# Performance work log

Hardware: AMD Instinct MI355X
Metric: run time of the kernel (lower is better)

The kernel has to match this reference:

```python
import jax, jax.numpy as jnp
import numpy as np

B, V, H, W, C = 2, 4, 120, 160, 96
N_VOX = 200000
GRID = 128
VOXEL_SIZE = 0.05
DEPTH_MIN = 0.1 / VOXEL_SIZE   # 2.0 (voxel units)
DEPTH_MAX = 4.0 / VOXEL_SIZE   # 80.0 (voxel units)
STEP = 0.5                     # ray increment = voxel_size/2, in voxel units
N_STEPS = int((DEPTH_MAX - DEPTH_MIN) / STEP)  # 156


def setup_inputs() -> dict:
    key = jax.random.key(0)
    kf, kc = jax.random.split(key)
    feats = jax.random.normal(kf, (B, V, H, W, C), dtype=jnp.float32)
    # batch-sorted sparse voxel coords [N,4] = (b, x, y, z)
    xyz = jax.random.randint(kc, (N_VOX, 3), 0, GRID).astype(jnp.int32)
    bcol = jnp.repeat(jnp.arange(B, dtype=jnp.int32), N_VOX // B)[:, None]
    coords = jnp.concatenate([bcol, xyz], axis=1)
    # camera-to-world matrices in voxel units: identity rotation (looking along +z),
    # cameras at z=0 spread across x so rays sweep the grid in depth range [2, 80]
    vm = np.tile(np.eye(4, dtype=np.float32), (B, V, 1, 1))
    vm[:, :, 0, 3] = np.array([40.0, 56.0, 72.0, 88.0], dtype=np.float32)[None, :]
    vm[:, :, 1, 3] = 64.0
    vm[:, :, 2, 3] = 0.0
    view_matrix = jnp.asarray(vm)
    intrinsic_params = jnp.array([80.0, 80.0, 80.0, 60.0], dtype=jnp.float32)  # fx,fy,cx,cy
    return {"encoded_2d_features": feats, "coords": coords,
            "view_matrix": view_matrix, "intrinsic_params": intrinsic_params}


def _project(encoded_2d_features, coords, view_matrix, intrinsic_params):
    n = coords.shape[0]
    # --- per-batch coordinate shift (as in original forward) ---
    local = coords[:, 1:]
    lc = local
    local_views = view_matrix
    for b in range(B):
        m = (coords[:, 0] == b)[:, None]
        shift = jnp.min(jnp.where(m, local, jnp.iinfo(jnp.int32).max), axis=0)  # [3]
        lc = jnp.where(m, lc - shift, lc)
        local_views = local_views.at[b, :, :3, 3].add(-shift.astype(view_matrix.dtype))
    # --- dense occupancy grid, permuted to [b, z, y, x]; -1 marks empty ---
    occ = jnp.full((B, GRID, GRID, GRID), -1, dtype=jnp.int32)
    occ = occ.at[coords[:, 0], lc[:, 2], lc[:, 1], lc[:, 0]].set(
        jnp.arange(n, dtype=jnp.int32))
    # --- per-pixel ray marching ---
    fx, fy, cx, cy = intrinsic_params
    t = DEPTH_MIN + STEP * jnp.arange(N_STEPS, dtype=jnp.float32)        # [S]
    dx = (jnp.arange(W, dtype=jnp.float32) + 0.5 - cx) / fx              # [W]
    dy = (jnp.arange(H, dtype=jnp.float32) + 0.5 - cy) / fy              # [H]
    # camera-space sample points along each pixel ray: [H, W, S, 3]
    pc = jnp.stack(jnp.broadcast_arrays(
        dx[None, :, None] * t, dy[:, None, None] * t,
        jnp.broadcast_to(t, (H, W, N_STEPS))), axis=-1)
    Rm = local_views[:, :, :3, :3]   # [B,V,3,3]
    tr = local_views[:, :, :3, 3]    # [B,V,3]
    # world (grid) space points: [B, V, H, W, S, 3]
    pw = jnp.einsum('bvij,hwsj->bvhwsi', Rm, pc) + tr[:, :, None, None, None, :]
    vox = jnp.floor(pw).astype(jnp.int32)
    ix, iy, iz = vox[..., 0], vox[..., 1], vox[..., 2]
    inb = ((ix >= 0) & (ix < GRID) & (iy >= 0) & (iy < GRID) &
           (iz >= 0) & (iz < GRID))
    bidx = jnp.arange(B, dtype=jnp.int32)[:, None, None, None, None]
    occ_val = occ[bidx,
                  jnp.clip(iz, 0, GRID - 1),
                  jnp.clip(iy, 0, GRID - 1),
                  jnp.clip(ix, 0, GRID - 1)]
    vox_id = jnp.where(inb, occ_val, -1)                                  # [B,V,H,W,S]
    # first occupied voxel hit along each ray
    hit = vox_id >= 0
    first = jnp.argmax(hit, axis=-1)                                      # [B,V,H,W]
    has_hit = jnp.any(hit, axis=-1)
    hit_id = jnp.take_along_axis(vox_id, first[..., None], axis=-1)[..., 0]
    tgt = jnp.where(has_hit, hit_id, n).reshape(-1)   # index n = dump slot for misses
    # scatter-accumulate pixel features into voxel slots + per-voxel counts
    flat_feat = encoded_2d_features.reshape(-1, C)
    proj = jnp.zeros((n + 1, C), dtype=encoded_2d_features.dtype).at[tgt].add(flat_feat)[:n]
    cnt = jnp.zeros((n + 1,), dtype=jnp.int32).at[tgt].add(1)[:n]
    out = proj / (cnt[:, None].astype(proj.dtype) + 1e-4)
    return out, cnt


def reference(encoded_2d_features, coords, view_matrix, intrinsic_params):
    return _project(encoded_2d_features, coords, view_matrix, intrinsic_params)
```

## Files before the change

### kernel.cpp

```cpp
#include <hip/hip_runtime.h>
#include <hip/hip_bf16.h>
#include <climits>

#define B_ 2
#define V_ 4
#define H_ 120
#define W_ 160
#define C_ 96
#define NVOX 200000
#define GRID_ 128
#define NSTEPS 156
#define NRAYS (B_*V_*H_*W_)
#define NB1 ((NVOX + 255) / 256)
#define CHUNK 64
#define OUTQ2 ((NVOX * C_) / 4)
#define NTHREADS_MARCH (2400 * 256)


__global__ void occ_kernel(const int* __restrict__ coords,
                           int* __restrict__ occ,
                           unsigned long long* __restrict__ mask) {
    int i = blockIdx.x * blockDim.x + threadIdx.x;
    if (i >= NVOX) return;
    int b = coords[i * 4 + 0];
    int x = coords[i * 4 + 1];
    int y = coords[i * 4 + 2];
    int z = coords[i * 4 + 3];
    int idx = ((b * GRID_ + z) * GRID_ + y) * GRID_ + x;
    atomicMax(&occ[idx], i);
    atomicOr(&mask[idx >> 6], 1ull << (idx & 63));
}

#define MARCH_COMPUTE(LIN, OK, W0)                                          \
    _Pragma("unroll")                                                       \
    for (int j = 0; j < 8; ++j) {                                           \
        int st = (W0) + sub * 8 + j;                                        \
        float t = 2.0f + 0.5f * (float)st;                                  \
        int ix = (int)floorf(d0 * t + t0);                                  \
        int iy = (int)floorf(d1 * t + t1);                                  \
        int iz = (int)floorf(d2 * t + t2);                                  \
        OK[j] = ((unsigned)ix < (unsigned)GRID_) &                          \
                ((unsigned)iy < (unsigned)GRID_) &                          \
                ((unsigned)iz < (unsigned)GRID_) & (st < NSTEPS);           \
        int cix = min(max(ix, 0), GRID_ - 1);                               \
        int ciy = min(max(iy, 0), GRID_ - 1);                               \
        int ciz = min(max(iz, 0), GRID_ - 1);                               \
        LIN[j] = vbase + (ciz << 14) + (ciy << 7) + cix;                    \
    }

#define MARCH_LOAD(U, LIN)                                                  \
    _Pragma("unroll")                                                       \
    for (int j = 0; j < 8; ++j) U[j] = mask[LIN[j] >> 6];

#define MARCH_EVAL(U, LIN, OK, W0)                                          \
    {                                                                       \
        int local = MISS;                                                   \
        _Pragma("unroll")                                                   \
        for (int j = 0; j < 8; ++j) {                                       \
            int st = (W0) + sub * 8 + j;                                    \
            if (OK[j] && ((U[j] >> (LIN[j] & 63)) & 1ull))                  \
                local = min(local, st);                                     \
        }                                                                   \
        local = min(local, __shfl_xor(local, 16));                          \
        local = min(local, __shfl_xor(local, 32));                          \
        if (local != MISS) { beststep = local; goto resolved; }             \
    }

__global__ void march_kernel(const float* __restrict__ vm,
                             const float* __restrict__ intr,
                             const unsigned long long* __restrict__ mask,
                             const int* __restrict__ occ,
                             int* __restrict__ tgt,
                             int* __restrict__ cnt,
                             float* __restrict__ out) {
    int gt   = blockIdx.x * blockDim.x + threadIdx.x;
    int lane = threadIdx.x & 63;
    int p    = lane & 15;
    int sub  = lane >> 4;
    int r    = ((gt >> 6) << 4) + p;
    {
        int w = r % W_;
        int h = (r / W_) % H_;
        int v = (r / (W_ * H_)) % V_;
        int b = r / (W_ * H_ * V_);
        const float* M = vm + (size_t)(b * V_ + v) * 16;
        float fx = intr[0], fy = intr[1], cx = intr[2], cy = intr[3];
        float dx = ((float)w + 0.5f - cx) / fx;
        float dy = ((float)h + 0.5f - cy) / fy;
        float d0 = M[0] * dx + M[1] * dy + M[2];
        float d1 = M[4] * dx + M[5] * dy + M[6];
        float d2 = M[8] * dx + M[9] * dy + M[10];
        float t0 = M[3];
        float t1 = M[7];
        float t2 = M[11];
        const int vbase = b * GRID_ * GRID_ * GRID_;
        const int MISS = 0x7FFFFFFF;
        int beststep = MISS;
        int res = -1;
        int linA[8], linB[8];
        bool okA[8], okB[8];
        unsigned long long uA[8], uB[8];
        MARCH_COMPUTE(linA, okA, 0)   MARCH_LOAD(uA, linA)
        MARCH_COMPUTE(linB, okB, 32)  MARCH_LOAD(uB, linB)
        MARCH_EVAL(uA, linA, okA, 0)
        MARCH_COMPUTE(linA, okA, 64)  MARCH_LOAD(uA, linA)
        MARCH_EVAL(uB, linB, okB, 32)
        MARCH_COMPUTE(linB, okB, 96)  MARCH_LOAD(uB, linB)
        MARCH_EVAL(uA, linA, okA, 64)
        MARCH_COMPUTE(linA, okA, 128) MARCH_LOAD(uA, linA)
        MARCH_EVAL(uB, linB, okB, 96)
        MARCH_EVAL(uA, linA, okA, 128)
resolved:
        if (sub == 0) {
            if (beststep != MISS) {
                float t = 2.0f + 0.5f * (float)beststep;
                int ix = (int)floorf(d0 * t + t0);
                int iy = (int)floorf(d1 * t + t1);
                int iz = (int)floorf(d2 * t + t2);
                res = occ[vbase + (iz << 14) + (iy << 7) + ix];
            }
            tgt[r] = res;
        }
        bool active = (sub == 0) && (res >= 0);
        int prevres = __shfl_up(res, 1);
        bool head = active && (p == 0 || prevres != res);
        bool boundary = head || !active;
        unsigned long long bb = __ballot(boundary);
        if (head) {
            unsigned long long above = bb & ~((2ull << lane) - 1);
            int next = above ? (__ffsll((long long)above) - 1) : 64;
            atomicAdd(&cnt[res], next - lane);
        }
    }
    float4 z4 = make_float4(0.f, 0.f, 0.f, 0.f);
    float4* o4 = (float4*)out;
    for (int i = gt; i < OUTQ2; i += NTHREADS_MARCH) o4[i] = z4;
}

__device__ __forceinline__ void flush_run(int t, int runlen, float ax, float ay,
                                          int lane,
                                          const int* __restrict__ cnt,
                                          float* __restrict__ out) {
    int c = cnt[t];
    float denom = (float)c + 0.0001f;
    if (runlen == c) {
        if (lane < 48) {
            float2 wv; wv.x = ax / denom; wv.y = ay / denom;
            ((float2*)(out + (size_t)t * C_))[lane] = wv;
        }
    } else if (lane < 48) {
        unsafeAtomicAdd(out + (size_t)t * C_ + 2 * lane,     ax / denom);
        unsafeAtomicAdd(out + (size_t)t * C_ + 2 * lane + 1, ay / denom);
    }
}

__global__ void scatter_kernel(const float* __restrict__ feats,
                               const int* __restrict__ tgt,
                               const int* __restrict__ cnt,
                               float* __restrict__ out,
                               float* __restrict__ cnt_out) {
    int gthread = blockIdx.x * blockDim.x + threadIdx.x;
    int lane = threadIdx.x & 63;
    for (int i = gthread; i < NVOX; i += NRAYS)
        cnt_out[i] = (float)cnt[i];
    int wave = gthread >> 6;
    int a = wave * CHUNK;
    int myt = tgt[a + lane];
    float ax = 0.0f, ay = 0.0f;
    int cur = -1, rstart = 0;
    for (int k0 = 0; k0 < CHUNK; k0 += 8) {
        float2 vbuf[8]; int tt[8];
#pragma unroll
        for (int j = 0; j < 8; ++j) {
            int k = k0 + j;
            tt[j] = __shfl(myt, k);
            vbuf[j] = make_float2(0.0f, 0.0f);
            if (tt[j] >= 0 && lane < 48)
                vbuf[j] = ((const float2*)(feats + (size_t)(a + k) * C_))[lane];
        }
#pragma unroll
        for (int j = 0; j < 8; ++j) {
            int k = k0 + j;
            if (tt[j] != cur) {
                if (cur >= 0) flush_run(cur, k - rstart, ax, ay, lane, cnt, out);
                cur = tt[j]; rstart = k; ax = 0.0f; ay = 0.0f;
            }
            ax += vbuf[j].x; ay += vbuf[j].y;
        }
    }
    if (cur >= 0) flush_run(cur, CHUNK - rstart, ax, ay, lane, cnt, out);
}

extern "C" void kernel_launch(void* const* d_in, const int* in_sizes, int n_in,
                              void* d_out, int out_size, void* d_ws, size_t ws_size,
                              hipStream_t stream) {
    const float* feats  = (const float*)d_in[0];
    const int*   coords = (const int*)d_in[1];
    const float* vm     = (const float*)d_in[2];
    const float* intr   = (const float*)d_in[3];

    float* out     = (float*)d_out;
    float* cnt_out = out + (size_t)NVOX * C_;

    char* ws = (char*)d_ws;
    int*                cnt  = (int*)(ws + 64);
    unsigned long long* mask = (unsigned long long*)(ws + 800064);
    int*  tgt = (int*)(ws + 1324416);
    int*  occ = (int*)(ws + 4786816);

    (void)hipMemsetAsync(ws, 0, 1324352, stream);

    occ_kernel<<<NB1, 256, 0, stream>>>(coords, occ, mask);
    march_kernel<<<2400, 256, 0, stream>>>(vm, intr, mask, occ, tgt, cnt, out);
    scatter_kernel<<<NRAYS / 256, 256, 0, stream>>>(feats, tgt, cnt, out, cnt_out);
}
```

Baseline: 187.7 us.

## Split output zeroing across kernels, dedupe mask loads, double-buffer scatter loads

Part of the output zero-fill (the first 1.6M float4s) moves into the small occ kernel, and the march kernel zeroes only the rest, so the march kernel carries less store traffic. The march mask loads reuse the previous 64-bit word when consecutive samples fall in the same word, which cuts redundant global loads. The scatter kernel's chunk loop is unrolled with two alternating register buffers so the next 8 feature loads are issued while the current 8 are consumed. This raises register pressure and code size in the scatter kernel, and the dependent select chain in the mask load may serialize those loads.

```diff
diff --git a/kernel.cpp b/kernel.cpp
--- a/kernel.cpp
+++ b/kernel.cpp
@@ -14,21 +14,29 @@
 #define NB1 ((NVOX + 255) / 256)
 #define CHUNK 64
 #define OUTQ2 ((NVOX * C_) / 4)
+#define ZOCC 1600000
+#define NTHREADS_OCC (NB1 * 256)
 #define NTHREADS_MARCH (2400 * 256)
 
 
 __global__ void occ_kernel(const int* __restrict__ coords,
                            int* __restrict__ occ,
-                           unsigned long long* __restrict__ mask) {
+                           unsigned long long* __restrict__ mask,
+                           float* __restrict__ out) {
     int i = blockIdx.x * blockDim.x + threadIdx.x;
-    if (i >= NVOX) return;
-    int b = coords[i * 4 + 0];
-    int x = coords[i * 4 + 1];
-    int y = coords[i * 4 + 2];
-    int z = coords[i * 4 + 3];
-    int idx = ((b * GRID_ + z) * GRID_ + y) * GRID_ + x;
-    atomicMax(&occ[idx], i);
-    atomicOr(&mask[idx >> 6], 1ull << (idx & 63));
+    if (i < NVOX) {
+        int b = coords[i * 4 + 0];
+        int x = coords[i * 4 + 1];
+        int y = coords[i * 4 + 2];
+        int z = coords[i * 4 + 3];
+        int idx = ((b * GRID_ + z) * GRID_ + y) * GRID_ + x;
+        atomicMax(&occ[idx], i);
+        atomicOr(&mask[idx >> 6], 1ull << (idx & 63));
+    }
+    float4 z4 = make_float4(0.f, 0.f, 0.f, 0.f);
+    float4* o4 = (float4*)out;
+    for (int q = blockIdx.x * blockDim.x + threadIdx.x; q < ZOCC; q += NTHREADS_OCC)
+        o4[q] = z4;
 }
 
 #define MARCH_COMPUTE(LIN, OK, W0)                                          \
@@ -49,8 +57,11 @@
     }
 
 #define MARCH_LOAD(U, LIN)                                                  \
-    _Pragma("unroll")                                                       \
-    for (int j = 0; j < 8; ++j) U[j] = mask[LIN[j] >> 6];
+    U[0] = mask[LIN[0] >> 6];                                               \
+    _Pragma("unroll")                                                       \
+    for (int j = 1; j < 8; ++j)                                             \
+        U[j] = ((LIN[j] >> 6) == (LIN[j - 1] >> 6)) ? U[j - 1]              \
+                                                    : mask[LIN[j] >> 6];
 
 #define MARCH_EVAL(U, LIN, OK, W0)                                          \
     {                                                                       \
@@ -134,7 +145,7 @@
     }
     float4 z4 = make_float4(0.f, 0.f, 0.f, 0.f);
     float4* o4 = (float4*)out;
-    for (int i = gt; i < OUTQ2; i += NTHREADS_MARCH) o4[i] = z4;
+    for (int i = ZOCC + gt; i < OUTQ2; i += NTHREADS_MARCH) o4[i] = z4;
 }
 
 __device__ __forceinline__ void flush_run(int t, int runlen, float ax, float ay,
@@ -154,6 +165,26 @@
     }
 }
 
+#define SC_LOAD(V, T, BASE)                                                 \
+    _Pragma("unroll")                                                       \
+    for (int j = 0; j < 8; ++j) {                                           \
+        T[j] = __shfl(myt, (BASE) + j);                                     \
+        V[j] = make_float2(0.0f, 0.0f);                                     \
+        if (T[j] >= 0 && lane < 48)                                         \
+            V[j] = ((const float2*)(feats + (size_t)(a + (BASE) + j) * C_))[lane]; \
+    }
+
+#define SC_CONSUME(V, T, BASE)                                              \
+    _Pragma("unroll")                                                       \
+    for (int j = 0; j < 8; ++j) {                                           \
+        int k = (BASE) + j;                                                 \
+        if (T[j] != cur) {                                                  \
+            if (cur >= 0) flush_run(cur, k - rstart, ax, ay, lane, cnt, out); \
+            cur = T[j]; rstart = k; ax = 0.0f; ay = 0.0f;                   \
+        }                                                                   \
+        ax += V[j].x; ay += V[j].y;                                         \
+    }
+
 __global__ void scatter_kernel(const float* __restrict__ feats,
                                const int* __restrict__ tgt,
                                const int* __restrict__ cnt,
@@ -168,26 +199,23 @@
     int myt = tgt[a + lane];
     float ax = 0.0f, ay = 0.0f;
     int cur = -1, rstart = 0;
-    for (int k0 = 0; k0 < CHUNK; k0 += 8) {
-        float2 vbuf[8]; int tt[8];
-#pragma unroll
-        for (int j = 0; j < 8; ++j) {
-            int k = k0 + j;
-            tt[j] = __shfl(myt, k);
-            vbuf[j] = make_float2(0.0f, 0.0f);
-            if (tt[j] >= 0 && lane < 48)
-                vbuf[j] = ((const float2*)(feats + (size_t)(a + k) * C_))[lane];
-        }
-#pragma unroll
-        for (int j = 0; j < 8; ++j) {
-            int k = k0 + j;
-            if (tt[j] != cur) {
-                if (cur >= 0) flush_run(cur, k - rstart, ax, ay, lane, cnt, out);
-                cur = tt[j]; rstart = k; ax = 0.0f; ay = 0.0f;
-            }
-            ax += vbuf[j].x; ay += vbuf[j].y;
-        }
-    }
+    float2 vA[8], vB[8]; int tA[8], tB[8];
+    SC_LOAD(vA, tA, 0)
+    SC_LOAD(vB, tB, 8)
+    SC_CONSUME(vA, tA, 0)
+    SC_LOAD(vA, tA, 16)
+    SC_CONSUME(vB, tB, 8)
+    SC_LOAD(vB, tB, 24)
+    SC_CONSUME(vA, tA, 16)
+    SC_LOAD(vA, tA, 32)
+    SC_CONSUME(vB, tB, 24)
+    SC_LOAD(vB, tB, 40)
+    SC_CONSUME(vA, tA, 32)
+    SC_LOAD(vA, tA, 48)
+    SC_CONSUME(vB, tB, 40)
+    SC_LOAD(vB, tB, 56)
+    SC_CONSUME(vA, tA, 48)
+    SC_CONSUME(vB, tB, 56)
     if (cur >= 0) flush_run(cur, CHUNK - rstart, ax, ay, lane, cnt, out);
 }
 
@@ -210,7 +238,7 @@
 
     (void)hipMemsetAsync(ws, 0, 1324352, stream);
 
-    occ_kernel<<<NB1, 256, 0, stream>>>(coords, occ, mask);
+    occ_kernel<<<NB1, 256, 0, stream>>>(coords, occ, mask, out);
     march_kernel<<<2400, 256, 0, stream>>>(vm, intr, mask, occ, tgt, cnt, out);
     scatter_kernel<<<NRAYS / 256, 256, 0, stream>>>(feats, tgt, cnt, out, cnt_out);
 }
```

Result: slower. 195.7 us (+4.2%).
